# Optimization experiments

Hardware: AMD Instinct MI355X
Metric: run time of the kernel (lower is better)

## Reference

```python
import jax, jax.numpy as jnp
import numpy as np

N_NODES, N_EDGES, BATCH, F_IN, GENES = 65536, 262144, 2048, 78, 735
HEADS, HID = 8, 64            # gnn_out_dim = HEADS*HID = 512
GOUT = HEADS * HID
NEG_SLOPE = 0.2
BN_EPS = 1e-5


def setup_inputs() -> dict:
    key = jax.random.key(0)
    ks = jax.random.split(key, 24)
    sc = lambda k, shp, fan: (jax.random.normal(k, shp, jnp.float32) / np.sqrt(fan)).astype(jnp.float32)
    d = {}
    d["x"] = jax.random.normal(ks[0], (N_NODES, F_IN), jnp.float32)
    d["edge_index"] = jax.random.randint(ks[1], (2, N_EDGES), 0, N_NODES)
    d["batch"] = jnp.sort(jax.random.randint(ks[2], (N_NODES,), 0, BATCH))
    d["x_gen"] = jax.random.normal(ks[3], (BATCH, GENES), jnp.float32)
    # GATConv 1: in=78 -> heads*hid
    d["W1"] = sc(ks[4], (F_IN, GOUT), F_IN)
    d["att_src1"] = sc(ks[5], (HEADS, HID), HID)
    d["att_dst1"] = sc(ks[6], (HEADS, HID), HID)
    d["bias1"] = jnp.zeros((GOUT,), jnp.float32)
    # GATConv 2: in=512 -> heads*hid
    d["W2"] = sc(ks[7], (GOUT, GOUT), GOUT)
    d["att_src2"] = sc(ks[8], (HEADS, HID), HID)
    d["att_dst2"] = sc(ks[9], (HEADS, HID), HID)
    d["bias2"] = jnp.zeros((GOUT,), jnp.float32)
    # geno encoder: Linear(735,128) -> BN -> ReLU -> Linear(128,512) -> ReLU
    d["gW1"] = sc(ks[10], (GENES, 2 * HID), GENES)
    d["gb1"] = jnp.zeros((2 * HID,), jnp.float32)
    d["bn_gamma"] = jnp.ones((2 * HID,), jnp.float32)
    d["bn_beta"] = jnp.zeros((2 * HID,), jnp.float32)
    d["bn_mean"] = jnp.zeros((2 * HID,), jnp.float32)
    d["bn_var"] = jnp.ones((2 * HID,), jnp.float32)
    d["gW2"] = sc(ks[11], (2 * HID, GOUT), 2 * HID)
    d["gb2"] = jnp.zeros((GOUT,), jnp.float32)
    # fusion MLP: 1024 -> 256 -> 128 -> 1
    d["fW1"] = sc(ks[12], (2 * GOUT, 256), 2 * GOUT)
    d["fb1"] = jnp.zeros((256,), jnp.float32)
    d["fW2"] = sc(ks[13], (256, 128), 256)
    d["fb2"] = jnp.zeros((128,), jnp.float32)
    d["fW3"] = sc(ks[14], (128, 1), 128)
    d["fb3"] = jnp.zeros((1,), jnp.float32)
    return d


def gat_layer(x, edge_index, W, att_src, att_dst, bias):
    """PyG GATConv (concat=True, add_self_loops=True), eval mode (no dropout)."""
    N = x.shape[0]
    H, C = att_src.shape
    h = (x @ W).reshape(N, H, C)                      # [N,H,C]
    a_src = jnp.einsum('nhc,hc->nh', h, att_src)      # [N,H]
    a_dst = jnp.einsum('nhc,hc->nh', h, att_dst)      # [N,H]
    loop = jnp.arange(N)
    src = jnp.concatenate([edge_index[0], loop])      # [E+N]
    dst = jnp.concatenate([edge_index[1], loop])
    e = jax.nn.leaky_relu(a_src[src] + a_dst[dst], NEG_SLOPE)   # [E+N,H]
    # scatter-softmax over incoming edges per destination node
    e_max = jax.ops.segment_max(e, dst, num_segments=N)
    e = jnp.exp(e - e_max[dst])
    denom = jax.ops.segment_sum(e, dst, num_segments=N)
    alpha = e / (denom[dst] + 1e-16)                  # [E+N,H]
    msg = h[src] * alpha[:, :, None]                  # [E+N,H,C]
    out = jax.ops.segment_sum(msg, dst, num_segments=N)  # [N,H,C]
    return out.reshape(N, H * C) + bias


def global_mean_pool(x, batch, num_graphs):
    sums = jax.ops.segment_sum(x, batch, num_segments=num_graphs)
    cnt = jax.ops.segment_sum(jnp.ones((x.shape[0],), x.dtype), batch, num_segments=num_graphs)
    return sums / jnp.maximum(cnt, 1.0)[:, None]


def reference(x, edge_index, batch, x_gen,
              W1, att_src1, att_dst1, bias1,
              W2, att_src2, att_dst2, bias2,
              gW1, gb1, bn_gamma, bn_beta, bn_mean, bn_var, gW2, gb2,
              fW1, fb1, fW2, fb2, fW3, fb3):
    h = jax.nn.elu(gat_layer(x, edge_index, W1, att_src1, att_dst1, bias1))
    h = jax.nn.elu(gat_layer(h, edge_index, W2, att_src2, att_dst2, bias2))
    g = global_mean_pool(h, batch, BATCH)             # [B, 512]
    # genomic encoder (eval-mode BatchNorm with running stats)
    z = x_gen @ gW1 + gb1
    z = (z - bn_mean) * jax.lax.rsqrt(bn_var + BN_EPS) * bn_gamma + bn_beta
    z = jax.nn.relu(z)
    z = jax.nn.relu(z @ gW2 + gb2)                    # [B, 512]
    c = jnp.concatenate([g, z], axis=1)               # [B, 1024]
    c = jax.nn.relu(c @ fW1 + fb1)
    c = jax.nn.relu(c @ fW2 + fb2)
    return c @ fW3 + fb3                              # [B, 1]
```

## Files before the change

### kernel.cpp

```cpp
#include <hip/hip_runtime.h>
#include <hip/hip_bf16.h>
#include <cstdint>
#include <cstddef>

#define NN 65536
#define NE 262144
#define NB 2048
#define FIN 78
#define GOUTD 512

typedef __bf16 bf16x8 __attribute__((ext_vector_type(8)));
typedef float f32x4 __attribute__((ext_vector_type(4)));

__device__ __forceinline__ float leaky02(float x) { return x > 0.f ? x : 0.2f * x; }
__device__ __forceinline__ void atomAddF(float* p, float v) { unsafeAtomicAdd(p, v); }

__global__ void k_hist(const int* __restrict__ dst, int* __restrict__ deg) {
    int i = blockIdx.x * 256 + threadIdx.x;
    if (i < NE) atomicAdd(&deg[dst[i]], 1);
}

__global__ void k_scan_block(const int* __restrict__ deg, int* __restrict__ ex, int* __restrict__ bsum) {
    __shared__ int s[256];
    int t = threadIdx.x; int g = blockIdx.x * 256 + t;
    int v = deg[g];
    s[t] = v; __syncthreads();
    for (int d = 1; d < 256; d <<= 1) {
        int x = (t >= d) ? s[t - d] : 0;
        __syncthreads();
        s[t] += x;
        __syncthreads();
    }
    ex[g] = s[t] - v;
    if (t == 255) bsum[blockIdx.x] = s[t];
}

__global__ void k_scan_add2(int* __restrict__ rowptr, const int* __restrict__ bsum) {
    __shared__ int s[256];
    int t = threadIdx.x;
    int v = bsum[t];
    s[t] = v; __syncthreads();
    for (int d = 1; d < 256; d <<= 1) {
        int x = (t >= d) ? s[t - d] : 0;
        __syncthreads();
        s[t] += x;
        __syncthreads();
    }
    int prefix = (blockIdx.x == 0) ? 0 : s[blockIdx.x - 1];
    int i = blockIdx.x * 256 + t;
    rowptr[i] += prefix;
    if (i == 0) rowptr[NN] = NE;
}

__global__ void k_scatter(const int* __restrict__ src, const int* __restrict__ dst,
                          const int* __restrict__ rowptr, int* __restrict__ fill,
                          int* __restrict__ colI) {
    int i = blockIdx.x * 256 + threadIdx.x;
    if (i < NE) {
        int d = dst[i];
        int pos = rowptr[d] + atomicAdd(&fill[d], 1);
        colI[pos] = src[i];
    }
}

__global__ void k_cvt_prep(const float* __restrict__ x, const float* __restrict__ W1,
                           const float* __restrict__ W2, __hip_bfloat16* __restrict__ xb,
                           __hip_bfloat16* __restrict__ w1t, __hip_bfloat16* __restrict__ w2t,
                           int* __restrict__ deg, int* __restrict__ fill,
                           const int* __restrict__ batch, int* __restrict__ gstart)
{
    int blk = blockIdx.x;
    if (blk < 16384) {
        int i = blk * 256 + threadIdx.x;
        int row = i >> 6;
        int c = (i & 63) << 1;
        float v0 = (c < FIN) ? x[(size_t)row * FIN + c] : 0.f;
        float v1 = (c + 1 < FIN) ? x[(size_t)row * FIN + c + 1] : 0.f;
        __hip_bfloat16 o[2];
        o[0] = __float2bfloat16(v0);
        o[1] = __float2bfloat16(v1);
        *(uint32_t*)&xb[(size_t)row * 128 + c] = *(const uint32_t*)o;
    } else if (blk < 16640) {
        int i = (blk - 16384) * 256 + threadIdx.x;
        int n = i >> 7, k = i & 127;
        w1t[i] = __float2bfloat16(k < FIN ? W1[(size_t)k * 512 + n] : 0.f);
    } else if (blk < 17664) {
        int i = (blk - 16640) * 256 + threadIdx.x;
        int n = i >> 9, k = i & 511;
        w2t[i] = __float2bfloat16(W2[(size_t)k * 512 + n]);
    } else {
        int i = (blk - 17664) * 256 + threadIdx.x;
        if (i < NN) {
            deg[i] = 0; fill[i] = 0;
            int cur = batch[i];
            int prev = (i == 0) ? -1 : batch[i - 1];
            for (int g = prev + 1; g <= cur; ++g) gstart[g] = i;
            if (i == NN - 1) {
                for (int g = cur + 1; g <= NB; ++g) gstart[g] = NN;
            }
        }
    }
}

__global__ __launch_bounds__(512) void k_mfma_gemm(
    const __hip_bfloat16* __restrict__ A, const __hip_bfloat16* __restrict__ BT,
    __hip_bfloat16* __restrict__ C, int K,
    const float* __restrict__ att_src, const float* __restrict__ att_dst,
    float* __restrict__ a_src, float* __restrict__ a_dst,
    float* __restrict__ t1, float* __restrict__ t2,
    const float* __restrict__ fb1, const float* __restrict__ fb2,
    float* __restrict__ z1)
{
    __shared__ __hip_bfloat16 smem[128 * 64 + 256 * 64];
    __hip_bfloat16* As = smem;
    __hip_bfloat16* Bs = smem + 128 * 64;
    int tid = threadIdx.x;
    int lane = tid & 63;
    int wave = tid >> 6;
    int wr = wave >> 2;
    int wc = wave & 3;
    int id = blockIdx.x;
    int m0 = (((id >> 4) << 3) + (id & 7)) * 128;
    int n0 = ((id >> 3) & 1) * 256;
    int wm = wr * 64;
    int wn = wc * 64;
    f32x4 acc[4][4] = {};

    int swz = lane & 7;

    for (int k0 = 0; k0 < K; k0 += 64) {
        #pragma unroll
        for (int c = 0; c < 2; ++c) {
            int off = c * 8192 + tid * 16;
            int r = off >> 7;
            int c16 = (off >> 4) & 7;
            int c16s = c16 ^ (r & 7);
            __builtin_amdgcn_global_load_lds(
                (const __attribute__((address_space(1))) void*)(A + (size_t)(m0 + r) * K + k0 + c16s * 8),
                (__attribute__((address_space(3))) void*)((char*)As + off), 16, 0, 0);
        }
        #pragma unroll
        for (int c = 0; c < 4; ++c) {
            int off = c * 8192 + tid * 16;
            int r = off >> 7;
            int c16 = (off >> 4) & 7;
            int c16s = c16 ^ (r & 7);
            __builtin_amdgcn_global_load_lds(
                (const __attribute__((address_space(1))) void*)(BT + (size_t)(n0 + r) * K + k0 + c16s * 8),
                (__attribute__((address_space(3))) void*)((char*)Bs + off), 16, 0, 0);
        }
        __syncthreads();
        #pragma unroll
        for (int kk = 0; kk < 64; kk += 32) {
            int c16r = (kk >> 3) + (lane >> 4);
            bf16x8 af[4], bfr[4];
            #pragma unroll
            for (int t = 0; t < 4; ++t) {
                int ra = wm + t * 16 + (lane & 15);
                int rb = wn + t * 16 + (lane & 15);
                af[t]  = *(const bf16x8*)((char*)As + ra * 128 + ((c16r ^ swz) << 4));
                bfr[t] = *(const bf16x8*)((char*)Bs + rb * 128 + ((c16r ^ swz) << 4));
            }
            #pragma unroll
            for (int i = 0; i < 4; ++i)
                #pragma unroll
                for (int j = 0; j < 4; ++j)
                    acc[i][j] = __builtin_amdgcn_mfma_f32_16x16x32_bf16(af[i], bfr[j], acc[i][j], 0, 0, 0);
        }
        __syncthreads();
    }

    #pragma unroll
    for (int p = 0; p < 2; ++p) {
        if ((wc >> 1) == p) {
            int rowb = wm + ((lane >> 4) << 2);
            int colb = (wc & 1) * 64 + (lane & 15);
            #pragma unroll
            for (int i = 0; i < 4; ++i) {
                #pragma unroll
                for (int j = 0; j < 4; ++j) {
                    int cc = colb + j * 16;
                    #pragma unroll
                    for (int r = 0; r < 4; ++r) {
                        int rr = rowb + i * 16 + r;
                        int word = (cc >> 1) ^ (((rr >> 2) & 7) << 3);
                        smem[rr * 128 + word * 2 + (cc & 1)] = __float2bfloat16(acc[i][j][r]);
                    }
                }
            }
        }
        __syncthreads();
        int cb = n0 + p * 128;
        #pragma unroll
        for (int cc2 = 0; cc2 < 4; ++cc2) {
            int pi = cc2 * 512 + tid;
            int rr = pi >> 4;
            int c16 = pi & 15;
            int x = ((rr >> 2) & 7) << 3;
            bf16x8 v = *(const bf16x8*)((char*)smem + rr * 256 + ((((c16 << 2) ^ x)) << 2));
            *(bf16x8*)(C + (size_t)(m0 + rr) * 512 + cb + c16 * 8) = v;
            const float* sp = att_src + cb + c16 * 8;
            const float* dp = att_dst + cb + c16 * 8;
            float4 s0 = *(const float4*)sp, s1 = *(const float4*)(sp + 4);
            float4 d0 = *(const float4*)dp, d1 = *(const float4*)(dp + 4);
            float sv[8] = {s0.x, s0.y, s0.z, s0.w, s1.x, s1.y, s1.z, s1.w};
            float dv[8] = {d0.x, d0.y, d0.z, d0.w, d1.x, d1.y, d1.z, d1.w};
            float ps = 0.f, pd = 0.f;
            #pragma unroll
            for (int k = 0; k < 8; ++k) {
                float f = (float)v[k];
                ps = fmaf(f, sv[k], ps);
                pd = fmaf(f, dv[k], pd);
            }
            #pragma unroll
            for (int d = 1; d < 8; d <<= 1) {
                ps += __shfl_xor(ps, d);
                pd += __shfl_xor(pd, d);
            }
            if ((c16 & 7) == 0) {
                int head = (cb >> 6) + (c16 >> 3);
                a_src[(size_t)(m0 + rr) * 8 + head] = ps;
                a_dst[(size_t)(m0 + rr) * 8 + head] = pd;
            }
        }
        __syncthreads();
    }

    if (t1) {
        if (tid < 128) {
            int r = 2 * id + (tid >> 6), e = tid & 63;
            *(float4*)(t1 + (size_t)r * 256 + e * 4) = *(const float4*)(fb1 + e * 4);
        } else if (tid < 192) {
            int q = tid - 128, r = 2 * id + (q >> 5), e = q & 31;
            *(float4*)(t2 + (size_t)r * 128 + e * 4) = *(const float4*)(fb2 + e * 4);
        } else if (tid < 256) {
            int q = tid - 192, r = 2 * id + (q >> 5), e = q & 31;
            *(float4*)(z1 + (size_t)r * 128 + e * 4) = make_float4(0.f, 0.f, 0.f, 0.f);
        }
    }
}

__global__ __launch_bounds__(256) void k_gat_agg(
    const __hip_bfloat16* __restrict__ h, const float* __restrict__ asrc,
    const float* __restrict__ adst, const int* __restrict__ rowptr,
    const int* __restrict__ colI, const float* __restrict__ bias,
    __hip_bfloat16* __restrict__ out)
{
    int lane = threadIdx.x & 63;
    int n = blockIdx.x * 4 + (threadIdx.x >> 6);
    int start = rowptr[n], end = rowptr[n + 1];
    int hh = lane >> 3;
    float adst_h = adst[n * 8 + hh];
    float acc[8];
    float wsum;
    {
        float w = __expf(leaky02(asrc[n * 8 + hh] + adst_h));
        wsum = w;
        bf16x8 v = *(const bf16x8*)(h + (size_t)n * GOUTD + lane * 8);
        #pragma unroll
        for (int j = 0; j < 8; ++j) acc[j] = w * (float)v[j];
    }
    int i = start;
    for (; i + 1 < end; i += 2) {
        int s0 = colI[i];
        int s1 = colI[i + 1];
        float w0 = __expf(leaky02(asrc[s0 * 8 + hh] + adst_h));
        float w1 = __expf(leaky02(asrc[s1 * 8 + hh] + adst_h));
        bf16x8 v0 = *(const bf16x8*)(h + (size_t)s0 * GOUTD + lane * 8);
        bf16x8 v1 = *(const bf16x8*)(h + (size_t)s1 * GOUTD + lane * 8);
        wsum += w0 + w1;
        #pragma unroll
        for (int j = 0; j < 8; ++j)
            acc[j] = fmaf(w0, (float)v0[j], fmaf(w1, (float)v1[j], acc[j]));
    }
    if (i < end) {
        int s = colI[i];
        float w = __expf(leaky02(asrc[s * 8 + hh] + adst_h));
        wsum += w;
        bf16x8 v = *(const bf16x8*)(h + (size_t)s * GOUTD + lane * 8);
        #pragma unroll
        for (int j = 0; j < 8; ++j) acc[j] = fmaf(w, (float)v[j], acc[j]);
    }
    float rden = 1.f / (wsum + 1e-16f);
    const float* bp = bias + lane * 8;
    float4 b0 = *(const float4*)bp, b1 = *(const float4*)(bp + 4);
    float bb[8] = {b0.x, b0.y, b0.z, b0.w, b1.x, b1.y, b1.z, b1.w};
    __hip_bfloat16 o[8] __attribute__((aligned(16)));
    #pragma unroll
    for (int j = 0; j < 8; ++j) {
        float v = fmaf(acc[j], rden, bb[j]);
        v = (v > 0.f) ? v : (__expf(v) - 1.f);
        o[j] = __float2bfloat16(v);
    }
    *(bf16x8*)(out + (size_t)n * GOUTD + lane * 8) = *(const bf16x8*)o;
}

__global__ __launch_bounds__(256) void k_gat_agg_pool(
    const __hip_bfloat16* __restrict__ h, const float* __restrict__ asrc,
    const float* __restrict__ adst, const int* __restrict__ rowptr,
    const int* __restrict__ colI, const float* __restrict__ bias,
    const int* __restrict__ gstart, float* __restrict__ cfeat)
{
    __shared__ float red[4][512];
    int lane = threadIdx.x & 63;
    int wv = threadIdx.x >> 6;
    int g = blockIdx.x;
    int s = gstart[g], e = gstart[g + 1];
    int hh = lane >> 3;
    const float* bp = bias + lane * 8;
    float4 b0 = *(const float4*)bp, b1 = *(const float4*)(bp + 4);
    float bb[8] = {b0.x, b0.y, b0.z, b0.w, b1.x, b1.y, b1.z, b1.w};
    float psum[8] = {};
    for (int n = s + wv; n < e; n += 4) {
        int start = rowptr[n], end = rowptr[n + 1];
        float adst_h = adst[n * 8 + hh];
        float acc[8];
        float wsum;
        {
            float w = __expf(leaky02(asrc[n * 8 + hh] + adst_h));
            wsum = w;
            bf16x8 v = *(const bf16x8*)(h + (size_t)n * GOUTD + lane * 8);
            #pragma unroll
            for (int j = 0; j < 8; ++j) acc[j] = w * (float)v[j];
        }
        int i = start;
        for (; i + 1 < end; i += 2) {
            int s0 = colI[i];
            int s1 = colI[i + 1];
            float w0 = __expf(leaky02(asrc[s0 * 8 + hh] + adst_h));
            float w1 = __expf(leaky02(asrc[s1 * 8 + hh] + adst_h));
            bf16x8 v0 = *(const bf16x8*)(h + (size_t)s0 * GOUTD + lane * 8);
            bf16x8 v1 = *(const bf16x8*)(h + (size_t)s1 * GOUTD + lane * 8);
            wsum += w0 + w1;
            #pragma unroll
            for (int j = 0; j < 8; ++j)
                acc[j] = fmaf(w0, (float)v0[j], fmaf(w1, (float)v1[j], acc[j]));
        }
        if (i < end) {
            int si = colI[i];
            float w = __expf(leaky02(asrc[si * 8 + hh] + adst_h));
            wsum += w;
            bf16x8 v = *(const bf16x8*)(h + (size_t)si * GOUTD + lane * 8);
            #pragma unroll
            for (int j = 0; j < 8; ++j) acc[j] = fmaf(w, (float)v[j], acc[j]);
        }
        float rden = 1.f / (wsum + 1e-16f);
        #pragma unroll
        for (int j = 0; j < 8; ++j) {
            float v = fmaf(acc[j], rden, bb[j]);
            v = (v > 0.f) ? v : (__expf(v) - 1.f);
            psum[j] += v;
        }
    }
    #pragma unroll
    for (int j = 0; j < 8; ++j) red[wv][lane * 8 + j] = psum[j];
    __syncthreads();
    if (wv == 0) {
        float inv = 1.f / fmaxf((float)(e - s), 1.f);
        float* cp = cfeat + (size_t)g * 1024;
        #pragma unroll
        for (int j = 0; j < 8; ++j) {
            int c = lane * 8 + j;
            cp[c] = (red[0][c] + red[1][c] + red[2][c] + red[3][c]) * inv;
        }
    }
}

__global__ __launch_bounds__(256) void k_geno1_sk(
    const float* __restrict__ A, const float* __restrict__ B, float* __restrict__ z1)
{
    __shared__ float As[32][34];
    __shared__ float Bs[32][68];
    int tid = threadIdx.x;
    int n0 = blockIdx.x * 64;
    int m0 = blockIdx.y * 32;
    int kbase = blockIdx.z * 192;
    int am = tid >> 3;
    int ak = (tid & 7) << 2;
    int bk = tid >> 4;
    int bc = (tid & 15) << 2;
    int tm = (tid >> 4) << 1;
    int tn = (tid & 15) << 2;
    float acc[2][4] = {};
    for (int kt = 0; kt < 192; kt += 32) {
        const float* ap = A + (size_t)(m0 + am) * 735 + kbase + kt + ak;
        int kg = kbase + kt + ak;
        As[ak][am]     = (kg     < 735) ? ap[0] : 0.f;
        As[ak + 1][am] = (kg + 1 < 735) ? ap[1] : 0.f;
        As[ak + 2][am] = (kg + 2 < 735) ? ap[2] : 0.f;
        As[ak + 3][am] = (kg + 3 < 735) ? ap[3] : 0.f;
        #pragma unroll
        for (int j = 0; j < 2; ++j) {
            int kr = j * 16 + bk;
            int kgb = kbase + kt + kr;
            float4 b4 = (kgb < 735) ? *(const float4*)(B + (size_t)kgb * 128 + n0 + bc)
                                    : make_float4(0.f, 0.f, 0.f, 0.f);
            *(float4*)&Bs[kr][bc] = b4;
        }
        __syncthreads();
        #pragma unroll
        for (int kk = 0; kk < 32; ++kk) {
            float2 a2 = *(const float2*)&As[kk][tm];
            float4 b4 = *(const float4*)&Bs[kk][tn];
            acc[0][0] = fmaf(a2.x, b4.x, acc[0][0]); acc[0][1] = fmaf(a2.x, b4.y, acc[0][1]);
            acc[0][2] = fmaf(a2.x, b4.z, acc[0][2]); acc[0][3] = fmaf(a2.x, b4.w, acc[0][3]);
            acc[1][0] = fmaf(a2.y, b4.x, acc[1][0]); acc[1][1] = fmaf(a2.y, b4.y, acc[1][1]);
            acc[1][2] = fmaf(a2.y, b4.z, acc[1][2]); acc[1][3] = fmaf(a2.y, b4.w, acc[1][3]);
        }
        __syncthreads();
    }
    #pragma unroll
    for (int i = 0; i < 2; ++i) {
        float* cp = z1 + (size_t)(m0 + tm + i) * 128 + n0 + tn;
        #pragma unroll
        for (int j = 0; j < 4; ++j) atomAddF(cp + j, acc[i][j]);
    }
}

__global__ __launch_bounds__(256) void k_geno2(
    const float* __restrict__ z1, const float* __restrict__ gW2,
    const float* __restrict__ gb1, const float* __restrict__ bn_mean,
    const float* __restrict__ bn_var, const float* __restrict__ bn_gamma,
    const float* __restrict__ bn_beta, const float* __restrict__ gb2,
    float* __restrict__ Cout)
{
    __shared__ float As[32][34];
    __shared__ float Bs[32][68];
    int tid = threadIdx.x;
    int n0 = blockIdx.x * 64;
    int m0 = blockIdx.y * 32;
    int am = tid >> 3;
    int ak = (tid & 7) << 2;
    int bk = tid >> 4;
    int bc = (tid & 15) << 2;
    int tm = (tid >> 4) << 1;
    int tn = (tid & 15) << 2;
    float acc[2][4] = {};
    for (int kt = 0; kt < 128; kt += 32) {
        int kg = kt + ak;
        float4 raw = *(const float4*)(z1 + (size_t)(m0 + am) * 128 + kg);
        float4 g1 = *(const float4*)(gb1 + kg);
        float4 mu = *(const float4*)(bn_mean + kg);
        float4 vr = *(const float4*)(bn_var + kg);
        float4 gm = *(const float4*)(bn_gamma + kg);
        float4 bt = *(const float4*)(bn_beta + kg);
        As[ak][am]     = fmaxf(fmaf(raw.x + g1.x - mu.x, rsqrtf(vr.x + 1e-5f) * gm.x, bt.x), 0.f);
        As[ak + 1][am] = fmaxf(fmaf(raw.y + g1.y - mu.y, rsqrtf(vr.y + 1e-5f) * gm.y, bt.y), 0.f);
        As[ak + 2][am] = fmaxf(fmaf(raw.z + g1.z - mu.z, rsqrtf(vr.z + 1e-5f) * gm.z, bt.z), 0.f);
        As[ak + 3][am] = fmaxf(fmaf(raw.w + g1.w - mu.w, rsqrtf(vr.w + 1e-5f) * gm.w, bt.w), 0.f);
        #pragma unroll
        for (int j = 0; j < 2; ++j) {
            int kr = j * 16 + bk;
            *(float4*)&Bs[kr][bc] = *(const float4*)(gW2 + (size_t)(kt + kr) * 512 + n0 + bc);
        }
        __syncthreads();
        #pragma unroll
        for (int kk = 0; kk < 32; ++kk) {
            float2 a2 = *(const float2*)&As[kk][tm];
            float4 b4 = *(const float4*)&Bs[kk][tn];
            acc[0][0] = fmaf(a2.x, b4.x, acc[0][0]); acc[0][1] = fmaf(a2.x, b4.y, acc[0][1]);
            acc[0][2] = fmaf(a2.x, b4.z, acc[0][2]); acc[0][3] = fmaf(a2.x, b4.w, acc[0][3]);
            acc[1][0] = fmaf(a2.y, b4.x, acc[1][0]); acc[1][1] = fmaf(a2.y, b4.y, acc[1][1]);
            acc[1][2] = fmaf(a2.y, b4.z, acc[1][2]); acc[1][3] = fmaf(a2.y, b4.w, acc[1][3]);
        }
        __syncthreads();
    }
    float4 bb = *(const float4*)(gb2 + n0 + tn);
    #pragma unroll
    for (int i = 0; i < 2; ++i) {
        float* cp = Cout + (size_t)(m0 + tm + i) * 1024 + n0 + tn;
        *(float4*)cp = make_float4(fmaxf(acc[i][0] + bb.x, 0.f), fmaxf(acc[i][1] + bb.y, 0.f),
                                   fmaxf(acc[i][2] + bb.z, 0.f), fmaxf(acc[i][3] + bb.w, 0.f));
    }
}

#define FBM 32
#define FBN 64
#define FKS 32

__global__ __launch_bounds__(256) void k_fgemm_sk(
    const float* __restrict__ A, const float* __restrict__ B,
    float* __restrict__ C, int N, int K, int KS, int reluA)
{
    __shared__ float As[FKS][FBM + 2];
    __shared__ float Bs[FKS][FBN + 4];
    int tid = threadIdx.x;
    int n0 = blockIdx.x * FBN;
    int m0 = blockIdx.y * FBM;
    int kbase = blockIdx.z * KS;
    int am = tid >> 3;
    int ak = (tid & 7) << 2;
    int bk = tid >> 4;
    int bc = (tid & 15) << 2;
    int tm = (tid >> 4) << 1;
    int tn = (tid & 15) << 2;
    float acc[2][4] = {};
    for (int kt = 0; kt < KS; kt += FKS) {
        float4 a4 = *(const float4*)(A + (size_t)(m0 + am) * K + kbase + kt + ak);
        if (reluA) {
            a4.x = fmaxf(a4.x, 0.f); a4.y = fmaxf(a4.y, 0.f);
            a4.z = fmaxf(a4.z, 0.f); a4.w = fmaxf(a4.w, 0.f);
        }
        As[ak][am] = a4.x; As[ak + 1][am] = a4.y;
        As[ak + 2][am] = a4.z; As[ak + 3][am] = a4.w;
        #pragma unroll
        for (int j = 0; j < 2; ++j) {
            int kr = j * 16 + bk;
            *(float4*)&Bs[kr][bc] = *(const float4*)(B + (size_t)(kbase + kt + kr) * N + n0 + bc);
        }
        __syncthreads();
        #pragma unroll
        for (int kk = 0; kk < FKS; ++kk) {
            float2 a2 = *(const float2*)&As[kk][tm];
            float4 b4 = *(const float4*)&Bs[kk][tn];
            acc[0][0] = fmaf(a2.x, b4.x, acc[0][0]); acc[0][1] = fmaf(a2.x, b4.y, acc[0][1]);
            acc[0][2] = fmaf(a2.x, b4.z, acc[0][2]); acc[0][3] = fmaf(a2.x, b4.w, acc[0][3]);
            acc[1][0] = fmaf(a2.y, b4.x, acc[1][0]); acc[1][1] = fmaf(a2.y, b4.y, acc[1][1]);
            acc[1][2] = fmaf(a2.y, b4.z, acc[1][2]); acc[1][3] = fmaf(a2.y, b4.w, acc[1][3]);
        }
        __syncthreads();
    }
    #pragma unroll
    for (int i = 0; i < 2; ++i) {
        float* cp = C + (size_t)(m0 + tm + i) * N + n0 + tn;
        #pragma unroll
        for (int j = 0; j < 4; ++j) atomAddF(cp + j, acc[i][j]);
    }
}

__global__ __launch_bounds__(256) void k_fout(
    const float* __restrict__ t2, const float* __restrict__ fW3,
    const float* __restrict__ fb3, float* __restrict__ out)
{
    int lane = threadIdx.x & 63;
    int row = blockIdx.x * 4 + (threadIdx.x >> 6);
    const float* tp = t2 + (size_t)row * 128;
    float p = fmaxf(tp[lane], 0.f) * fW3[lane] + fmaxf(tp[lane + 64], 0.f) * fW3[lane + 64];
    #pragma unroll
    for (int d = 1; d < 64; d <<= 1) p += __shfl_xor(p, d);
    if (lane == 0) out[row] = p + fb3[0];
}

extern "C" void kernel_launch(void* const* d_in, const int* in_sizes, int n_in,
                              void* d_out, int out_size, void* d_ws, size_t ws_size,
                              hipStream_t stream) {
    const float* x        = (const float*)d_in[0];
    const int*   ei       = (const int*)d_in[1];
    const int*   batch    = (const int*)d_in[2];
    const float* x_gen    = (const float*)d_in[3];
    const float* W1       = (const float*)d_in[4];
    const float* att_src1 = (const float*)d_in[5];
    const float* att_dst1 = (const float*)d_in[6];
    const float* bias1    = (const float*)d_in[7];
    const float* W2       = (const float*)d_in[8];
    const float* att_src2 = (const float*)d_in[9];
    const float* att_dst2 = (const float*)d_in[10];
    const float* bias2    = (const float*)d_in[11];
    const float* gW1      = (const float*)d_in[12];
    const float* gb1      = (const float*)d_in[13];
    const float* bn_gamma = (const float*)d_in[14];
    const float* bn_beta  = (const float*)d_in[15];
    const float* bn_mean  = (const float*)d_in[16];
    const float* bn_var   = (const float*)d_in[17];
    const float* gW2      = (const float*)d_in[18];
    const float* gb2      = (const float*)d_in[19];
    const float* fW1      = (const float*)d_in[20];
    const float* fb1      = (const float*)d_in[21];
    const float* fW2      = (const float*)d_in[22];
    const float* fb2      = (const float*)d_in[23];
    const float* fW3      = (const float*)d_in[24];
    const float* fb3      = (const float*)d_in[25];
    float* out = (float*)d_out;

    const int* srcv = ei;
    const int* dstv = ei + NE;

    char* w = (char*)d_ws;
    size_t off = 0;
    auto take = [&](size_t bytes) -> void* {
        void* p = w + off;
        off += (bytes + 255) & ~(size_t)255;
        return p;
    };
    __hip_bfloat16* hbuf = (__hip_bfloat16*)take((size_t)NN * GOUTD * 2);
    __hip_bfloat16* abuf = (__hip_bfloat16*)take((size_t)NN * GOUTD * 2);
    __hip_bfloat16* xb   = (__hip_bfloat16*)take((size_t)NN * 128 * 2);
    __hip_bfloat16* w1t  = (__hip_bfloat16*)take((size_t)512 * 128 * 2);
    __hip_bfloat16* w2t  = (__hip_bfloat16*)take((size_t)512 * 512 * 2);
    float* asrc   = (float*)take((size_t)NN * 8 * 4);
    float* adst   = (float*)take((size_t)NN * 8 * 4);
    int*   rowptr = (int*)take((size_t)(NN + 1) * 4);
    int*   colI   = (int*)take((size_t)NE * 4);
    int*   deg    = (int*)take((size_t)NN * 4);
    int*   fill   = (int*)take((size_t)NN * 4);
    int*   bsum   = (int*)take(256 * 4);
    int*   gstart = (int*)take((NB + 1) * 4);
    float* cbuf = (float*)xb;
    float* z1   = cbuf + (size_t)2048 * 1024;
    float* t1   = z1 + (size_t)2048 * 128;
    float* t2   = t1 + (size_t)2048 * 256;

    k_cvt_prep<<<17920, 256, 0, stream>>>(x, W1, W2, xb, w1t, w2t, deg, fill, batch, gstart);
    k_hist<<<NE / 256, 256, 0, stream>>>(dstv, deg);
    k_scan_block<<<256, 256, 0, stream>>>(deg, rowptr, bsum);
    k_scan_add2<<<256, 256, 0, stream>>>(rowptr, bsum);
    k_scatter<<<NE / 256, 256, 0, stream>>>(srcv, dstv, rowptr, fill, colI);

    k_mfma_gemm<<<1024, 512, 0, stream>>>(xb, w1t, hbuf, 128, att_src1, att_dst1, asrc, adst,
                                          nullptr, nullptr, nullptr, nullptr, nullptr);
    k_gat_agg<<<NN / 4, 256, 0, stream>>>(hbuf, asrc, adst, rowptr, colI, bias1, abuf);

    k_mfma_gemm<<<1024, 512, 0, stream>>>(abuf, w2t, hbuf, 512, att_src2, att_dst2, asrc, adst,
                                          t1, t2, fb1, fb2, z1);

    k_gat_agg_pool<<<NB, 256, 0, stream>>>(hbuf, asrc, adst, rowptr, colI, bias2,
                                           gstart, cbuf);

    k_geno1_sk<<<dim3(2, 64, 4), 256, 0, stream>>>(x_gen, gW1, z1);
    k_geno2<<<dim3(8, 64), 256, 0, stream>>>(z1, gW2, gb1, bn_mean, bn_var, bn_gamma,
                                             bn_beta, gb2, cbuf + 512);

    k_fgemm_sk<<<dim3(4, 64, 4), 256, 0, stream>>>(cbuf, fW1, t1, 256, 1024, 256, 0);
    k_fgemm_sk<<<dim3(2, 64, 4), 256, 0, stream>>>(t1, fW2, t2, 128, 256, 64, 1);
    k_fout<<<NB / 4, 256, 0, stream>>>(t2, fW3, fb3, out);
}
```

Before: 438.6 us.

## Fuse CSR scatter into layer-1 GEMM launch with dedicated 128x128-tile kernel

Adds a specialized layer-1 GEMM kernel that uses 256-thread blocks with 128x128 tiles and a swizzled LDS epilogue that also computes the attention logits. The same launch runs the edge-scatter work for CSR construction in extra blocks, so one kernel launch is removed and the scatter overlaps with the GEMM. The x-to-bf16 conversion also now reads a float2 vector load instead of two scalar loads. This adds a second GEMM code path to maintain, and the scatter blocks compete with the GEMM blocks for the same compute units.

```diff
diff --git a/kernel.cpp b/kernel.cpp
--- a/kernel.cpp
+++ b/kernel.cpp
@@ -52,17 +52,6 @@
     if (i == 0) rowptr[NN] = NE;
 }
 
-__global__ void k_scatter(const int* __restrict__ src, const int* __restrict__ dst,
-                          const int* __restrict__ rowptr, int* __restrict__ fill,
-                          int* __restrict__ colI) {
-    int i = blockIdx.x * 256 + threadIdx.x;
-    if (i < NE) {
-        int d = dst[i];
-        int pos = rowptr[d] + atomicAdd(&fill[d], 1);
-        colI[pos] = src[i];
-    }
-}
-
 __global__ void k_cvt_prep(const float* __restrict__ x, const float* __restrict__ W1,
                            const float* __restrict__ W2, __hip_bfloat16* __restrict__ xb,
                            __hip_bfloat16* __restrict__ w1t, __hip_bfloat16* __restrict__ w2t,
@@ -74,11 +63,11 @@
         int i = blk * 256 + threadIdx.x;
         int row = i >> 6;
         int c = (i & 63) << 1;
-        float v0 = (c < FIN) ? x[(size_t)row * FIN + c] : 0.f;
-        float v1 = (c + 1 < FIN) ? x[(size_t)row * FIN + c + 1] : 0.f;
+        float2 v = (c < FIN) ? *(const float2*)(x + (size_t)row * FIN + c)
+                             : make_float2(0.f, 0.f);
         __hip_bfloat16 o[2];
-        o[0] = __float2bfloat16(v0);
-        o[1] = __float2bfloat16(v1);
+        o[0] = __float2bfloat16(v.x);
+        o[1] = __float2bfloat16(v.y);
         *(uint32_t*)&xb[(size_t)row * 128 + c] = *(const uint32_t*)o;
     } else if (blk < 16640) {
         int i = (blk - 16384) * 256 + threadIdx.x;
@@ -98,6 +87,123 @@
             if (i == NN - 1) {
                 for (int g = cur + 1; g <= NB; ++g) gstart[g] = NN;
             }
+        }
+    }
+}
+
+__global__ __launch_bounds__(256) void k_mfma_gemm1(
+    const __hip_bfloat16* __restrict__ A, const __hip_bfloat16* __restrict__ BT,
+    __hip_bfloat16* __restrict__ C, int K,
+    const float* __restrict__ att_src, const float* __restrict__ att_dst,
+    float* __restrict__ a_src, float* __restrict__ a_dst,
+    const int* __restrict__ srcv, const int* __restrict__ dstv,
+    const int* __restrict__ rowptr, int* __restrict__ fill, int* __restrict__ colI)
+{
+    if (blockIdx.x >= 2048) {
+        int i = (blockIdx.x - 2048) * 256 + threadIdx.x;
+        if (i < NE) {
+            int d = dstv[i];
+            int pos = rowptr[d] + atomicAdd(&fill[d], 1);
+            colI[pos] = srcv[i];
+        }
+        return;
+    }
+    __shared__ __hip_bfloat16 smem[128 * 128];
+    __hip_bfloat16* As = smem;
+    __hip_bfloat16* Bs = smem + 128 * 64;
+    int tid = threadIdx.x;
+    int lane = tid & 63;
+    int wave = tid >> 6;
+    int id = blockIdx.x;
+    int m0 = (((id >> 5) << 3) + (id & 7)) * 128;
+    int n0 = ((id >> 3) & 3) * 128;
+    int wm = (wave >> 1) * 64;
+    int wn = (wave & 1) * 64;
+    f32x4 acc[4][4] = {};
+
+    int swz = lane & 7;
+
+    for (int k0 = 0; k0 < K; k0 += 64) {
+        #pragma unroll
+        for (int c = 0; c < 4; ++c) {
+            int off = c * 4096 + tid * 16;
+            int r = off >> 7;
+            int c16 = (off >> 4) & 7;
+            int c16s = c16 ^ (r & 7);
+            __builtin_amdgcn_global_load_lds(
+                (const __attribute__((address_space(1))) void*)(A + (size_t)(m0 + r) * K + k0 + c16s * 8),
+                (__attribute__((address_space(3))) void*)((char*)As + off), 16, 0, 0);
+            __builtin_amdgcn_global_load_lds(
+                (const __attribute__((address_space(1))) void*)(BT + (size_t)(n0 + r) * K + k0 + c16s * 8),
+                (__attribute__((address_space(3))) void*)((char*)Bs + off), 16, 0, 0);
+        }
+        __syncthreads();
+        #pragma unroll
+        for (int kk = 0; kk < 64; kk += 32) {
+            int c16r = (kk >> 3) + (lane >> 4);
+            bf16x8 af[4], bfr[4];
+            #pragma unroll
+            for (int t = 0; t < 4; ++t) {
+                int ra = wm + t * 16 + (lane & 15);
+                int rb = wn + t * 16 + (lane & 15);
+                af[t]  = *(const bf16x8*)((char*)As + ra * 128 + ((c16r ^ swz) << 4));
+                bfr[t] = *(const bf16x8*)((char*)Bs + rb * 128 + ((c16r ^ swz) << 4));
+            }
+            #pragma unroll
+            for (int i = 0; i < 4; ++i)
+                #pragma unroll
+                for (int j = 0; j < 4; ++j)
+                    acc[i][j] = __builtin_amdgcn_mfma_f32_16x16x32_bf16(af[i], bfr[j], acc[i][j], 0, 0, 0);
+        }
+        __syncthreads();
+    }
+
+    int rowb = wm + ((lane >> 4) << 2);
+    int colb = wn + (lane & 15);
+    #pragma unroll
+    for (int i = 0; i < 4; ++i) {
+        #pragma unroll
+        for (int j = 0; j < 4; ++j) {
+            int cc = colb + j * 16;
+            #pragma unroll
+            for (int r = 0; r < 4; ++r) {
+                int rr = rowb + i * 16 + r;
+                int word = (cc >> 1) ^ (((rr >> 2) & 7) << 3);
+                smem[rr * 128 + word * 2 + (cc & 1)] = __float2bfloat16(acc[i][j][r]);
+            }
+        }
+    }
+    __syncthreads();
+    #pragma unroll
+    for (int cc2 = 0; cc2 < 8; ++cc2) {
+        int p = cc2 * 256 + tid;
+        int rr = p >> 4;
+        int c16 = p & 15;
+        int x = ((rr >> 2) & 7) << 3;
+        bf16x8 v = *(const bf16x8*)((char*)smem + rr * 256 + ((((c16 << 2) ^ x)) << 2));
+        *(bf16x8*)(C + (size_t)(m0 + rr) * 512 + n0 + c16 * 8) = v;
+        const float* sp = att_src + n0 + c16 * 8;
+        const float* dp = att_dst + n0 + c16 * 8;
+        float4 s0 = *(const float4*)sp, s1 = *(const float4*)(sp + 4);
+        float4 d0 = *(const float4*)dp, d1 = *(const float4*)(dp + 4);
+        float sv[8] = {s0.x, s0.y, s0.z, s0.w, s1.x, s1.y, s1.z, s1.w};
+        float dv[8] = {d0.x, d0.y, d0.z, d0.w, d1.x, d1.y, d1.z, d1.w};
+        float ps = 0.f, pd = 0.f;
+        #pragma unroll
+        for (int k = 0; k < 8; ++k) {
+            float f = (float)v[k];
+            ps = fmaf(f, sv[k], ps);
+            pd = fmaf(f, dv[k], pd);
+        }
+        #pragma unroll
+        for (int d = 1; d < 8; d <<= 1) {
+            ps += __shfl_xor(ps, d);
+            pd += __shfl_xor(pd, d);
+        }
+        if ((c16 & 7) == 0) {
+            int head = (n0 >> 6) + (c16 >> 3);
+            a_src[(size_t)(m0 + rr) * 8 + head] = ps;
+            a_dst[(size_t)(m0 + rr) * 8 + head] = pd;
         }
     }
 }
@@ -604,10 +710,9 @@
     k_hist<<<NE / 256, 256, 0, stream>>>(dstv, deg);
     k_scan_block<<<256, 256, 0, stream>>>(deg, rowptr, bsum);
     k_scan_add2<<<256, 256, 0, stream>>>(rowptr, bsum);
-    k_scatter<<<NE / 256, 256, 0, stream>>>(srcv, dstv, rowptr, fill, colI);
-
-    k_mfma_gemm<<<1024, 512, 0, stream>>>(xb, w1t, hbuf, 128, att_src1, att_dst1, asrc, adst,
-                                          nullptr, nullptr, nullptr, nullptr, nullptr);
+
+    k_mfma_gemm1<<<3072, 256, 0, stream>>>(xb, w1t, hbuf, 128, att_src1, att_dst1, asrc, adst,
+                                           srcv, dstv, rowptr, fill, colI);
     k_gat_agg<<<NN / 4, 256, 0, stream>>>(hbuf, asrc, adst, rowptr, colI, bias1, abuf);
 
     k_mfma_gemm<<<1024, 512, 0, stream>>>(abuf, w2t, hbuf, 512, att_src2, att_dst2, asrc, adst,
```

Measured after the change: 433.5 us. About the same (-1.2%).
